# Kernel tuning notes

Hardware: AMD Instinct MI355X
Metric: run time of the kernel (lower is better)

Reference implementation:

```python
import jax, jax.numpy as jnp
import numpy as np

BATCH = 4096
DIM = 512
TEMP = 0.5
EPS = 1e-8


def setup_inputs() -> dict:
    key = jax.random.key(0)
    k1, k2 = jax.random.split(key)
    z_i = jax.random.normal(k1, (BATCH, DIM), dtype=jnp.float32)
    z_j = jax.random.normal(k2, (BATCH, DIM), dtype=jnp.float32)
    return {"z_i": z_i, "z_j": z_j}


def reference(z_i, z_j):
    N = z_i.shape[0]
    temperature = jnp.asarray(TEMP, z_i.dtype)
    z = jnp.concatenate([z_i, z_j], axis=0)  # [2N, D]
    # cosine similarity = (x . y) / max(||x||*||y||, eps), as torch CosineSimilarity
    norms = jnp.sqrt(jnp.sum(z * z, axis=-1, keepdims=True))  # [2N, 1]
    dots = z @ z.T                                            # [2N, 2N]
    denom = jnp.maximum(norms * norms.T, EPS)
    sim = dots / denom / temperature                          # [2N, 2N]

    idx = jnp.arange(2 * N)
    # positive pair: offset +N / -N diagonals == partner index (i+N) mod 2N
    pos = sim[idx, (idx + N) % (2 * N)]                       # [2N]
    # CE with label 0 over logits [pos, negatives]: the full candidate set per
    # row is every sim entry except the self-diagonal (positive included once).
    masked = jnp.where(jnp.eye(2 * N, dtype=bool), -jnp.inf, sim)
    lse = jax.nn.logsumexp(masked, axis=1)                    # [2N]
    loss = jnp.sum(lse - pos) / (2 * N)
    return loss
```

## Files before the change

### kernel.cpp

```cpp
#include <hip/hip_runtime.h>


#define NROWS 8192
#define HALF_N 4096
#define KD 512
#define TILE 128
#define BK 128
#define NT (NROWS / TILE)

typedef unsigned char u8;
typedef __attribute__((ext_vector_type(4))) int i32x4;
typedef __attribute__((ext_vector_type(8))) int i32x8;
typedef __attribute__((ext_vector_type(4))) float f32x4;

__device__ inline void load16_to_lds(const u8* g, u8* l) {
  __builtin_amdgcn_global_load_lds((const __attribute__((address_space(1))) void*)g,
                                   (__attribute__((address_space(3))) void*)l,
                                   16, 0, 0);
}

__global__ __launch_bounds__(256) void nt_normalize(const float* __restrict__ zi,
                                                    const float* __restrict__ zj,
                                                    u8* __restrict__ zq,
                                                    float* __restrict__ rowsum,
                                                    float* __restrict__ possum,
                                                    float* __restrict__ out) {
  const int t = threadIdx.x;
  if (t < 4) rowsum[blockIdx.x * 4 + t] = 0.f;
  if (blockIdx.x == 0 && t == 4) { possum[0] = 0.f; out[0] = 0.f; }

  const int wave = t >> 6, lane = t & 63;
  const int row = blockIdx.x * 4 + wave;
  const float* src = (row < HALF_N) ? (zi + (size_t)row * KD)
                                    : (zj + (size_t)(row - HALF_N) * KD);
  const float4 v0 = ((const float4*)src)[lane * 2];
  const float4 v1 = ((const float4*)src)[lane * 2 + 1];
  float ss = v0.x * v0.x + v0.y * v0.y + v0.z * v0.z + v0.w * v0.w +
             v1.x * v1.x + v1.y * v1.y + v1.z * v1.z + v1.w * v1.w;
#pragma unroll
  for (int m = 1; m < 64; m <<= 1) ss += __shfl_xor(ss, m);
  const float inv = rsqrtf(ss);
  int lo = __builtin_amdgcn_cvt_pk_fp8_f32(v0.x * inv, v0.y * inv, 0, false);
  lo = __builtin_amdgcn_cvt_pk_fp8_f32(v0.z * inv, v0.w * inv, lo, true);
  int hi = __builtin_amdgcn_cvt_pk_fp8_f32(v1.x * inv, v1.y * inv, 0, false);
  hi = __builtin_amdgcn_cvt_pk_fp8_f32(v1.z * inv, v1.w * inv, hi, true);
  ((int2*)(zq + (size_t)row * KD))[lane] = make_int2(lo, hi);
}

__global__ __launch_bounds__(256) void nt_gemm(const u8* __restrict__ zq,
                                               float* __restrict__ rowsum,
                                               float* __restrict__ possum) {
  __shared__ __attribute__((aligned(16))) u8 lA[TILE * BK];
  __shared__ __attribute__((aligned(16))) u8 lB[TILE * BK];
  __shared__ float lrow[TILE];
  __shared__ float lcol[TILE];

  const int bid = blockIdx.x;
  int tm = (int)((float)(2 * NT + 1) * 0.5f -
                 sqrtf((float)(2 * NT + 1) * (float)(2 * NT + 1) * 0.25f - 2.0f * (float)bid));
  if (tm < 0) tm = 0;
  if (tm > NT - 1) tm = NT - 1;
  while ((tm + 1) * NT - ((tm + 1) * tm) / 2 <= bid) ++tm;
  while (tm * NT - (tm * (tm - 1)) / 2 > bid) --tm;
  const int tn = tm + (bid - (tm * NT - (tm * (tm - 1)) / 2));
  const bool diag = (tm == tn);
  const bool isPos = (tn - tm == 32);

  const int t = threadIdx.x;
  const int wave = t >> 6, lane = t & 63;
  const int wm = wave >> 1, wn = wave & 1;
  const int c16 = lane & 15, quad = lane >> 4;

  const int rowA = tm * TILE, rowB = tn * TILE;

  f32x4 acc[4][4] = {};

  const u8* Bt = diag ? lA : lB;
  const int q2 = quad * 2;

  for (int k0 = 0; k0 < KD; k0 += BK) {
    __syncthreads();
#pragma unroll
    for (int it = 0; it < 4; ++it) {
      const int chunk = it * 256 + t;
      const int r = chunk >> 3, cpos = chunk & 7;
      const int c = cpos ^ (r & 7);
      u8* dstA = &lA[(it * 256 + wave * 64) * 16];
      load16_to_lds(&zq[(size_t)(rowA + r) * KD + k0 + c * 16], dstA);
      if (!diag) {
        u8* dstB = &lB[(it * 256 + wave * 64) * 16];
        load16_to_lds(&zq[(size_t)(rowB + r) * KD + k0 + c * 16], dstB);
      }
    }
    __syncthreads();

    i32x8 bg[4];
#pragma unroll
    for (int ni = 0; ni < 4; ++ni) {
      const int rB = wn * 64 + ni * 16 + c16;
      const i32x4 bl = *(const i32x4*)&Bt[(rB * 8 + (q2 ^ (rB & 7))) * 16];
      const i32x4 bh = *(const i32x4*)&Bt[(rB * 8 + ((q2 + 1) ^ (rB & 7))) * 16];
      bg[ni] = (i32x8){bl[0], bl[1], bl[2], bl[3], bh[0], bh[1], bh[2], bh[3]};
    }
#pragma unroll
    for (int mi = 0; mi < 4; ++mi) {
      const int rA = wm * 64 + mi * 16 + c16;
      const i32x4 al = *(const i32x4*)&lA[(rA * 8 + (q2 ^ (rA & 7))) * 16];
      const i32x4 ah = *(const i32x4*)&lA[(rA * 8 + ((q2 + 1) ^ (rA & 7))) * 16];
      const i32x8 af = (i32x8){al[0], al[1], al[2], al[3], ah[0], ah[1], ah[2], ah[3]};
#pragma unroll
      for (int ni = 0; ni < 4; ++ni)
        acc[mi][ni] = __builtin_amdgcn_mfma_scale_f32_16x16x128_f8f6f4(
            af, bg[ni], acc[mi][ni],
            0, 0,
            0, 0x7F7F7F7F,
            0, 0x7F7F7F7F);
    }
  }

  const bool ownDiag = (quad == (c16 >> 2));
  const int rdiag = c16 & 3;

  if (isPos && wm == wn) {
    float p = 0.f;
    if (ownDiag) {
#pragma unroll
      for (int mi = 0; mi < 4; ++mi) p += acc[mi][mi][rdiag];
    }
#pragma unroll
    for (int m = 1; m < 64; m <<= 1) p += __shfl_xor(p, m);
    if (lane == 0) atomicAdd(possum, 4.0f * p);
  }

#pragma unroll
  for (int mi = 0; mi < 4; ++mi)
#pragma unroll
    for (int ni = 0; ni < 4; ++ni)
#pragma unroll
      for (int r = 0; r < 4; ++r)
        acc[mi][ni][r] = __expf(2.0f * acc[mi][ni][r]);

  if (diag && wm == wn && ownDiag) {
#pragma unroll
    for (int mi = 0; mi < 4; ++mi) acc[mi][mi][rdiag] = 0.f;
  }

  if (t < TILE) { lrow[t] = 0.f; lcol[t] = 0.f; }
  __syncthreads();

#pragma unroll
  for (int mi = 0; mi < 4; ++mi) {
#pragma unroll
    for (int r = 0; r < 4; ++r) {
      float e = acc[mi][0][r] + acc[mi][1][r] + acc[mi][2][r] + acc[mi][3][r];
      e += __shfl_xor(e, 1);
      e += __shfl_xor(e, 2);
      e += __shfl_xor(e, 4);
      e += __shfl_xor(e, 8);
      if (c16 == 0) atomicAdd(&lrow[wm * 64 + mi * 16 + quad * 4 + r], e);
    }
  }
  if (!diag) {
#pragma unroll
    for (int ni = 0; ni < 4; ++ni) {
      float g = 0.f;
#pragma unroll
      for (int mi = 0; mi < 4; ++mi)
#pragma unroll
        for (int r = 0; r < 4; ++r) g += acc[mi][ni][r];
      g += __shfl_xor(g, 16);
      g += __shfl_xor(g, 32);
      if (quad == 0) atomicAdd(&lcol[wn * 64 + ni * 16 + c16], g);
    }
  }
  __syncthreads();
  if (t < TILE) {
    atomicAdd(&rowsum[rowA + t], lrow[t]);
    if (!diag) atomicAdd(&rowsum[rowB + t], lcol[t]);
  }
}

__global__ __launch_bounds__(256) void nt_finalize(const float* __restrict__ rowsum,
                                                   const float* __restrict__ possum,
                                                   float* __restrict__ out) {
  const int t = threadIdx.x;
  const int i = blockIdx.x * 256 + t;
  float v = logf(rowsum[i]);
#pragma unroll
  for (int m = 1; m < 64; m <<= 1) v += __shfl_xor(v, m);
  __shared__ float bsum[4];
  if ((t & 63) == 0) bsum[t >> 6] = v;
  __syncthreads();
  if (t == 0) {
    float s = bsum[0] + bsum[1] + bsum[2] + bsum[3];
    if (blockIdx.x == 0) s -= possum[0];
    atomicAdd(out, s * (1.0f / NROWS));
  }
}

extern "C" void kernel_launch(void* const* d_in, const int* in_sizes, int n_in,
                              void* d_out, int out_size, void* d_ws, size_t ws_size,
                              hipStream_t stream) {
  const float* zi = (const float*)d_in[0];
  const float* zj = (const float*)d_in[1];
  float* out = (float*)d_out;

  u8* zq = (u8*)d_ws;
  float* rowsum = (float*)((char*)d_ws + (size_t)NROWS * KD);
  float* possum = rowsum + NROWS;

  nt_normalize<<<NROWS / 4, 256, 0, stream>>>(zi, zj, zq, rowsum, possum, out);
  nt_gemm<<<NT * (NT + 1) / 2, 256, 0, stream>>>(zq, rowsum, possum);
  nt_finalize<<<NROWS / 256, 256, 0, stream>>>(rowsum, possum, out);
}
```

Before: 109.9 us.

## Load GEMM operands directly from global memory into registers, dropping LDS staging

The fp8 GEMM kernel no longer stages A/B tiles through LDS with global_load_lds and barriers; each lane now reads its MFMA fragments straight from global memory with 16-byte vector loads, and the K loop is fully unrolled. This removes the LDS writes, the LDS reads and the per-iteration __syncthreads. Operand reuse across waves now relies on L1/L2 instead of shared memory, which raises global load traffic per block.

Measured after the change: 138.2 us. +25.8%, slower.

```diff
diff --git a/kernel.cpp b/kernel.cpp
--- a/kernel.cpp
+++ b/kernel.cpp
@@ -12,12 +12,6 @@
 typedef __attribute__((ext_vector_type(4))) int i32x4;
 typedef __attribute__((ext_vector_type(8))) int i32x8;
 typedef __attribute__((ext_vector_type(4))) float f32x4;
-
-__device__ inline void load16_to_lds(const u8* g, u8* l) {
-  __builtin_amdgcn_global_load_lds((const __attribute__((address_space(1))) void*)g,
-                                   (__attribute__((address_space(3))) void*)l,
-                                   16, 0, 0);
-}
 
 __global__ __launch_bounds__(256) void nt_normalize(const float* __restrict__ zi,
                                                     const float* __restrict__ zj,
@@ -50,8 +44,6 @@
 __global__ __launch_bounds__(256) void nt_gemm(const u8* __restrict__ zq,
                                                float* __restrict__ rowsum,
                                                float* __restrict__ possum) {
-  __shared__ __attribute__((aligned(16))) u8 lA[TILE * BK];
-  __shared__ __attribute__((aligned(16))) u8 lB[TILE * BK];
   __shared__ float lrow[TILE];
   __shared__ float lcol[TILE];
 
@@ -73,49 +65,41 @@
 
   const int rowA = tm * TILE, rowB = tn * TILE;
 
+  const u8* aptr[4];
+  const u8* bptr[4];
+#pragma unroll
+  for (int mi = 0; mi < 4; ++mi)
+    aptr[mi] = zq + (size_t)(rowA + wm * 64 + mi * 16 + c16) * KD + quad * 32;
+#pragma unroll
+  for (int ni = 0; ni < 4; ++ni)
+    bptr[ni] = zq + (size_t)(rowB + wn * 64 + ni * 16 + c16) * KD + quad * 32;
+
   f32x4 acc[4][4] = {};
 
-  const u8* Bt = diag ? lA : lB;
-  const int q2 = quad * 2;
-
+#pragma unroll
   for (int k0 = 0; k0 < KD; k0 += BK) {
-    __syncthreads();
+    i32x8 af[4], bg[4];
 #pragma unroll
-    for (int it = 0; it < 4; ++it) {
-      const int chunk = it * 256 + t;
-      const int r = chunk >> 3, cpos = chunk & 7;
-      const int c = cpos ^ (r & 7);
-      u8* dstA = &lA[(it * 256 + wave * 64) * 16];
-      load16_to_lds(&zq[(size_t)(rowA + r) * KD + k0 + c * 16], dstA);
-      if (!diag) {
-        u8* dstB = &lB[(it * 256 + wave * 64) * 16];
-        load16_to_lds(&zq[(size_t)(rowB + r) * KD + k0 + c * 16], dstB);
-      }
+    for (int mi = 0; mi < 4; ++mi) {
+      const i32x4 lo = *(const i32x4*)(aptr[mi] + k0);
+      const i32x4 hi = *(const i32x4*)(aptr[mi] + k0 + 16);
+      af[mi] = (i32x8){lo[0], lo[1], lo[2], lo[3], hi[0], hi[1], hi[2], hi[3]};
     }
-    __syncthreads();
-
-    i32x8 bg[4];
 #pragma unroll
     for (int ni = 0; ni < 4; ++ni) {
-      const int rB = wn * 64 + ni * 16 + c16;
-      const i32x4 bl = *(const i32x4*)&Bt[(rB * 8 + (q2 ^ (rB & 7))) * 16];
-      const i32x4 bh = *(const i32x4*)&Bt[(rB * 8 + ((q2 + 1) ^ (rB & 7))) * 16];
-      bg[ni] = (i32x8){bl[0], bl[1], bl[2], bl[3], bh[0], bh[1], bh[2], bh[3]};
+      const i32x4 lo = *(const i32x4*)(bptr[ni] + k0);
+      const i32x4 hi = *(const i32x4*)(bptr[ni] + k0 + 16);
+      bg[ni] = (i32x8){lo[0], lo[1], lo[2], lo[3], hi[0], hi[1], hi[2], hi[3]};
     }
 #pragma unroll
-    for (int mi = 0; mi < 4; ++mi) {
-      const int rA = wm * 64 + mi * 16 + c16;
-      const i32x4 al = *(const i32x4*)&lA[(rA * 8 + (q2 ^ (rA & 7))) * 16];
-      const i32x4 ah = *(const i32x4*)&lA[(rA * 8 + ((q2 + 1) ^ (rA & 7))) * 16];
-      const i32x8 af = (i32x8){al[0], al[1], al[2], al[3], ah[0], ah[1], ah[2], ah[3]};
+    for (int mi = 0; mi < 4; ++mi)
 #pragma unroll
       for (int ni = 0; ni < 4; ++ni)
         acc[mi][ni] = __builtin_amdgcn_mfma_scale_f32_16x16x128_f8f6f4(
-            af, bg[ni], acc[mi][ni],
+            af[mi], bg[ni], acc[mi][ni],
             0, 0,
             0, 0x7F7F7F7F,
             0, 0x7F7F7F7F);
-    }
   }
 
   const bool ownDiag = (quad == (c16 >> 2));
```

## Fuse normalize, GEMM and finalize into one kernel with per-tile flags

Applied to the files above, without the earlier changes.

Merges the three kernel launches into a single persistent-style kernel. The first block that needs a 128-row group normalizes and quantizes it, then publishes a release flag, while other blocks spin on that flag. The last block to finish, found with a global done counter, computes the log-sum and final loss. This removes two launch boundaries and the small finalize kernel, but adds a memset, spin-waiting that assumes claimant blocks make forward progress, and serialized normalization inside the early tiles.

Result: slower. 354.4 us (+222.5%).

```diff
diff --git a/kernel.cpp b/kernel.cpp
--- a/kernel.cpp
+++ b/kernel.cpp
@@ -7,6 +7,7 @@
 #define TILE 128
 #define BK 128
 #define NT (NROWS / TILE)
+#define NTILES (NT * (NT + 1) / 2)
 
 typedef unsigned char u8;
 typedef __attribute__((ext_vector_type(4))) int i32x4;
@@ -19,41 +20,49 @@
                                    16, 0, 0);
 }
 
-__global__ __launch_bounds__(256) void nt_normalize(const float* __restrict__ zi,
-                                                    const float* __restrict__ zj,
-                                                    u8* __restrict__ zq,
-                                                    float* __restrict__ rowsum,
-                                                    float* __restrict__ possum,
-                                                    float* __restrict__ out) {
-  const int t = threadIdx.x;
-  if (t < 4) rowsum[blockIdx.x * 4 + t] = 0.f;
-  if (blockIdx.x == 0 && t == 4) { possum[0] = 0.f; out[0] = 0.f; }
-
-  const int wave = t >> 6, lane = t & 63;
-  const int row = blockIdx.x * 4 + wave;
-  const float* src = (row < HALF_N) ? (zi + (size_t)row * KD)
-                                    : (zj + (size_t)(row - HALF_N) * KD);
-  const float4 v0 = ((const float4*)src)[lane * 2];
-  const float4 v1 = ((const float4*)src)[lane * 2 + 1];
-  float ss = v0.x * v0.x + v0.y * v0.y + v0.z * v0.z + v0.w * v0.w +
-             v1.x * v1.x + v1.y * v1.y + v1.z * v1.z + v1.w * v1.w;
-#pragma unroll
-  for (int m = 1; m < 64; m <<= 1) ss += __shfl_xor(ss, m);
-  const float inv = rsqrtf(ss);
-  int lo = __builtin_amdgcn_cvt_pk_fp8_f32(v0.x * inv, v0.y * inv, 0, false);
-  lo = __builtin_amdgcn_cvt_pk_fp8_f32(v0.z * inv, v0.w * inv, lo, true);
-  int hi = __builtin_amdgcn_cvt_pk_fp8_f32(v1.x * inv, v1.y * inv, 0, false);
-  hi = __builtin_amdgcn_cvt_pk_fp8_f32(v1.z * inv, v1.w * inv, hi, true);
-  ((int2*)(zq + (size_t)row * KD))[lane] = make_int2(lo, hi);
-}
-
-__global__ __launch_bounds__(256) void nt_gemm(const u8* __restrict__ zq,
-                                               float* __restrict__ rowsum,
-                                               float* __restrict__ possum) {
+__device__ void norm_group(int g, const float* __restrict__ zi,
+                           const float* __restrict__ zj, u8* __restrict__ zq,
+                           float* __restrict__ rowsum, int* flag,
+                           int t, int wave, int lane) {
+  for (int r = wave; r < TILE; r += 4) {
+    const int row = g * TILE + r;
+    const float* src = (row < HALF_N) ? (zi + (size_t)row * KD)
+                                      : (zj + (size_t)(row - HALF_N) * KD);
+    const float4 v0 = ((const float4*)src)[lane * 2];
+    const float4 v1 = ((const float4*)src)[lane * 2 + 1];
+    float ss = v0.x * v0.x + v0.y * v0.y + v0.z * v0.z + v0.w * v0.w +
+               v1.x * v1.x + v1.y * v1.y + v1.z * v1.z + v1.w * v1.w;
+#pragma unroll
+    for (int m = 1; m < 64; m <<= 1) ss += __shfl_xor(ss, m);
+    const float inv = rsqrtf(ss);
+    int lo = __builtin_amdgcn_cvt_pk_fp8_f32(v0.x * inv, v0.y * inv, 0, false);
+    lo = __builtin_amdgcn_cvt_pk_fp8_f32(v0.z * inv, v0.w * inv, lo, true);
+    int hi = __builtin_amdgcn_cvt_pk_fp8_f32(v1.x * inv, v1.y * inv, 0, false);
+    hi = __builtin_amdgcn_cvt_pk_fp8_f32(v1.z * inv, v1.w * inv, hi, true);
+    ((int2*)(zq + (size_t)row * KD))[lane] = make_int2(lo, hi);
+  }
+  if (t < TILE) rowsum[g * TILE + t] = 0.f;
+  __syncthreads();
+  if (t == 0)
+    __hip_atomic_store(flag, 2, __ATOMIC_RELEASE, __HIP_MEMORY_SCOPE_AGENT);
+}
+
+__global__ __launch_bounds__(256) void nt_fused(const float* __restrict__ zi,
+                                                const float* __restrict__ zj,
+                                                u8* __restrict__ zq,
+                                                float* __restrict__ rowsum,
+                                                int* __restrict__ ctrl,
+                                                float* __restrict__ out) {
+  float* possum = (float*)ctrl;
+  int* done = ctrl + 1;
+  int* flags = ctrl + 2;
+
   __shared__ __attribute__((aligned(16))) u8 lA[TILE * BK];
   __shared__ __attribute__((aligned(16))) u8 lB[TILE * BK];
   __shared__ float lrow[TILE];
   __shared__ float lcol[TILE];
+  __shared__ int sclaim;
+  __shared__ int slast;
 
   const int bid = blockIdx.x;
   int tm = (int)((float)(2 * NT + 1) * 0.5f -
@@ -68,15 +77,34 @@
 
   const int t = threadIdx.x;
   const int wave = t >> 6, lane = t & 63;
+
+  if (t == 0) {
+    int c = 0;
+    if (atomicCAS(&flags[tm], 0, 1) == 0) c |= 1;
+    if (!diag && atomicCAS(&flags[tn], 0, 1) == 0) c |= 2;
+    sclaim = c;
+  }
+  __syncthreads();
+  if (sclaim & 1) norm_group(tm, zi, zj, zq, rowsum, &flags[tm], t, wave, lane);
+  if (sclaim & 2) norm_group(tn, zi, zj, zq, rowsum, &flags[tn], t, wave, lane);
+  if (t == 0) {
+    while (__hip_atomic_load(&flags[tm], __ATOMIC_ACQUIRE,
+                             __HIP_MEMORY_SCOPE_AGENT) != 2)
+      __builtin_amdgcn_s_sleep(8);
+    if (!diag)
+      while (__hip_atomic_load(&flags[tn], __ATOMIC_ACQUIRE,
+                               __HIP_MEMORY_SCOPE_AGENT) != 2)
+        __builtin_amdgcn_s_sleep(8);
+  }
+  __syncthreads();
+
   const int wm = wave >> 1, wn = wave & 1;
   const int c16 = lane & 15, quad = lane >> 4;
-
+  const int q2 = quad * 2;
   const int rowA = tm * TILE, rowB = tn * TILE;
+  const u8* Bt = diag ? lA : lB;
 
   f32x4 acc[4][4] = {};
-
-  const u8* Bt = diag ? lA : lB;
-  const int q2 = quad * 2;
 
   for (int k0 = 0; k0 < KD; k0 += BK) {
     __syncthreads();
@@ -178,23 +206,28 @@
     atomicAdd(&rowsum[rowA + t], lrow[t]);
     if (!diag) atomicAdd(&rowsum[rowB + t], lcol[t]);
   }
-}
-
-__global__ __launch_bounds__(256) void nt_finalize(const float* __restrict__ rowsum,
-                                                   const float* __restrict__ possum,
-                                                   float* __restrict__ out) {
-  const int t = threadIdx.x;
-  const int i = blockIdx.x * 256 + t;
-  float v = logf(rowsum[i]);
-#pragma unroll
-  for (int m = 1; m < 64; m <<= 1) v += __shfl_xor(v, m);
-  __shared__ float bsum[4];
-  if ((t & 63) == 0) bsum[t >> 6] = v;
+
   __syncthreads();
   if (t == 0) {
-    float s = bsum[0] + bsum[1] + bsum[2] + bsum[3];
-    if (blockIdx.x == 0) s -= possum[0];
-    atomicAdd(out, s * (1.0f / NROWS));
+    const int me = __hip_atomic_fetch_add(done, 1, __ATOMIC_ACQ_REL,
+                                          __HIP_MEMORY_SCOPE_AGENT);
+    slast = (me == NTILES - 1);
+  }
+  __syncthreads();
+  if (slast) {
+    float s = 0.f;
+    for (int i = t; i < NROWS; i += 256)
+      s += logf(__hip_atomic_load(&rowsum[i], __ATOMIC_RELAXED,
+                                  __HIP_MEMORY_SCOPE_AGENT));
+#pragma unroll
+    for (int m = 1; m < 64; m <<= 1) s += __shfl_xor(s, m);
+    if (lane == 0) lrow[wave] = s;
+    __syncthreads();
+    if (t == 0) {
+      const float ps = __hip_atomic_load(possum, __ATOMIC_RELAXED,
+                                         __HIP_MEMORY_SCOPE_AGENT);
+      out[0] = (lrow[0] + lrow[1] + lrow[2] + lrow[3] - ps) * (1.0f / NROWS);
+    }
   }
 }
 
@@ -207,9 +240,8 @@
 
   u8* zq = (u8*)d_ws;
   float* rowsum = (float*)((char*)d_ws + (size_t)NROWS * KD);
-  float* possum = rowsum + NROWS;
-
-  nt_normalize<<<NROWS / 4, 256, 0, stream>>>(zi, zj, zq, rowsum, possum, out);
-  nt_gemm<<<NT * (NT + 1) / 2, 256, 0, stream>>>(zq, rowsum, possum);
-  nt_finalize<<<NROWS / 256, 256, 0, stream>>>(rowsum, possum, out);
-}
+  int* ctrl = (int*)(rowsum + NROWS);
+
+  hipMemsetAsync(ctrl, 0, 66 * sizeof(int), stream);
+  nt_fused<<<NTILES, 256, 0, stream>>>(zi, zj, zq, rowsum, ctrl, out);
+}
```
